# Kernel tuning notes

Measured on AMD Instinct MI355X. Metric: run time of the kernel, lower is better.

The kernel has to match this reference:

```python
import jax, jax.numpy as jnp
import numpy as np

EMBED_DIM = 128
NUM_HEADS = 4
WH, WW = 7, 7
N = WH * WW
HEAD_DIM = EMBED_DIM // NUM_HEADS
SCALE = HEAD_DIM ** -0.5


def _rel_position_index():
    # double_step_seq(2*Ww-1, Wh, 1, Ww), then idx = coords + coords.T, flip cols
    seq1 = np.arange(0, (2 * WW - 1) * WH, 2 * WW - 1)
    seq2 = np.arange(0, WW)
    coords = (seq1[:, None] + seq2[None, :]).reshape(1, -1)  # (1, N)
    idx = coords + coords.T                                   # (N, N)
    idx = idx[:, ::-1].copy()                                 # flip(1)
    return jnp.asarray(idx, dtype=jnp.int32)

REL_IDX = _rel_position_index()


def setup_inputs() -> dict:
    key = jax.random.key(0)
    ks = jax.random.split(key, 8)
    B = 4096
    nW = 64
    C = EMBED_DIM
    x = jax.random.normal(ks[0], (B, N, C), dtype=jnp.float32)
    # shift mask: values in (-inf, 0]; emulate with -100 on ~half the entries
    mask = jnp.where(jax.random.uniform(ks[1], (nW, N, N)) > 0.5, -100.0, 0.0).astype(jnp.float32)
    lim = 1.0 / np.sqrt(C)
    qkv_w = jax.random.uniform(ks[2], (3 * C, C), minval=-lim, maxval=lim, dtype=jnp.float32)
    qkv_b = jax.random.uniform(ks[3], (3 * C,), minval=-lim, maxval=lim, dtype=jnp.float32)
    proj_w = jax.random.uniform(ks[4], (C, C), minval=-lim, maxval=lim, dtype=jnp.float32)
    proj_b = jax.random.uniform(ks[5], (C,), minval=-lim, maxval=lim, dtype=jnp.float32)
    n_rel = (2 * WH - 1) * (2 * WW - 1)
    bias_table = 0.02 * jax.random.normal(ks[6], (n_rel, NUM_HEADS), dtype=jnp.float32)
    return {"x": x, "mask": mask, "qkv_w": qkv_w, "qkv_b": qkv_b,
            "proj_w": proj_w, "proj_b": proj_b, "bias_table": bias_table}


def reference(x, mask, qkv_w, qkv_b, proj_w, proj_b, bias_table):
    B, n, C = x.shape
    H, D = NUM_HEADS, HEAD_DIM
    qkv = x @ qkv_w.T + qkv_b                       # (B, N, 3C)
    qkv = qkv.reshape(B, n, 3, H, D).transpose(2, 0, 3, 1, 4)
    q, k, v = qkv[0], qkv[1], qkv[2]                # each (B, H, N, D)
    attn = jnp.einsum('bhnd,bhmd->bhnm', q * SCALE, k)
    # relative position bias gather: (N, N, H) -> (H, N, N)
    rel_bias = bias_table[REL_IDX.reshape(-1)].reshape(n, n, H).transpose(2, 0, 1)
    attn = attn + rel_bias[None]
    nW = mask.shape[0]
    attn = attn.reshape(B // nW, nW, H, n, n) + mask[None, :, None]
    attn = attn.reshape(B, H, n, n)
    attn = jax.nn.softmax(attn, axis=-1)
    out = jnp.einsum('bhnm,bhmd->bhnd', attn, v)    # (B, H, N, D)
    out = out.transpose(0, 2, 1, 3).reshape(B, n, C)
    return out @ proj_w.T + proj_b
```

## Files before the change

### kernel.cpp

```cpp
#include <hip/hip_runtime.h>


typedef __bf16 bf16_t;
typedef __bf16 bf8v  __attribute__((ext_vector_type(8)));
typedef __bf16 bf4v  __attribute__((ext_vector_type(4)));
typedef float  f4v   __attribute__((ext_vector_type(4)));

#define QK_SCALE 0.17677669529663687f

__device__ __forceinline__ f4v mfma16(bf8v a, bf8v b, f4v c) {
  return __builtin_amdgcn_mfma_f32_16x16x32_bf16(a, b, c, 0, 0, 0);
}

__device__ __forceinline__ bf8v join8(bf4v lo, bf4v hi) {
  return __builtin_shufflevector(lo, hi, 0, 1, 2, 3, 4, 5, 6, 7);
}

__global__ void prep_kernel(const float* __restrict__ mask,
                            const float* __restrict__ qkv_w,
                            const float* __restrict__ proj_w,
                            const float* __restrict__ bias_table,
                            bf16_t* __restrict__ wq,
                            bf16_t* __restrict__ wp,
                            float* __restrict__ cbs) {
  const int stride = gridDim.x * blockDim.x;
  const int tid0 = blockIdx.x * blockDim.x + threadIdx.x;
  for (int i = tid0; i < 24 * 4 * 64 * 8; i += stride) {
    int j = i & 7, l = (i >> 3) & 63, kt = (i >> 9) & 3, t = i >> 11;
    int n = t * 16 + (l & 15), k = kt * 32 + (l >> 4) * 8 + j;
    wq[i] = (bf16_t)qkv_w[n * 128 + k];
  }
  for (int i = tid0; i < 8 * 4 * 64 * 8; i += stride) {
    int j = i & 7, l = (i >> 3) & 63, kt = (i >> 9) & 3, t = i >> 11;
    int n = t * 16 + (l & 15), k = kt * 32 + (l >> 4) * 8 + j;
    wp[i] = (bf16_t)proj_w[n * 128 + k];
  }
  for (int i = tid0; i < 64 * 4 * 64 * 64; i += stride) {
    int j = i & 63;
    int l16 = j >> 2, nt = j & 3;
    int m = nt * 16 + l16;
    int n = (i >> 6) & 63, h = (i >> 12) & 3, w = i >> 14;
    float v;
    if (m >= 49) {
      v = -1e30f;
    } else if (n >= 49) {
      v = 0.0f;
    } else {
      int cn = 13 * (n / 7) + n % 7;
      int mm = 48 - m;
      int cm = 13 * (mm / 7) + mm % 7;
      v = bias_table[(cn + cm) * 4 + h] + mask[(w * 49 + n) * 49 + m];
    }
    cbs[i] = v;
  }
}

__global__ __launch_bounds__(256, 3) void msa_kernel(
    const float* __restrict__ x,
    const float* __restrict__ qkv_b,
    const float* __restrict__ proj_b,
    const bf16_t* __restrict__ wq,
    const bf16_t* __restrict__ wp,
    const float* __restrict__ cbs,
    float* __restrict__ out) {
  __shared__ __align__(16) bf16_t gA[8704];
  __shared__ __align__(16) bf16_t gB[4][4608];

#define AS(r, c)   gA[(r) * 136 + (c)]
#define VT(h, d, t) gA[((h) * 32 + (d)) * 68 + (t)]
#define QQ(h, r, d) gB[h][(r) * 36 + (d)]
#define KK(h, r, d) gB[h][2304 + (r) * 36 + (d)]
#define PP(h, n, m) gB[h][(n) * 72 + (m)]
#define OV(h, t, d) gB[h][(t) * 36 + (d)]

  const int tid = threadIdx.x;
  const int wv  = tid >> 6;
  const int ln  = tid & 63;
  const int l16 = ln & 15;
  const int l4  = ln >> 4;
  const int b   = blockIdx.x;
  const int w   = b & 63;

  {
    const float4* xb = (const float4*)(x + (size_t)b * (49 * 128));
    for (int i = tid; i < 64 * 32; i += 256) {
      int r = i >> 5, c4 = (i & 31) << 2;
      float4 v;
      if (r < 49) v = xb[(r * 128 + c4) >> 2];
      else        v = make_float4(0.f, 0.f, 0.f, 0.f);
      bf4v o = { (bf16_t)v.x, (bf16_t)v.y, (bf16_t)v.z, (bf16_t)v.w };
      *(bf4v*)&AS(r, c4) = o;
    }
  }
  __syncthreads();

  {
    f4v acc[4][6];
    for (int mt = 0; mt < 4; ++mt)
      for (int nj = 0; nj < 6; ++nj) acc[mt][nj] = (f4v){0.f, 0.f, 0.f, 0.f};
    for (int kt = 0; kt < 4; ++kt) {
      bf8v a[4];
      for (int mt = 0; mt < 4; ++mt)
        a[mt] = *(const bf8v*)&AS(mt * 16 + l16, kt * 32 + l4 * 8);
      bf8v bwv[6];
      for (int nj = 0; nj < 6; ++nj) {
        int t = wv * 6 + nj;
        bwv[nj] = *(const bf8v*)(wq + (((t * 4 + kt) * 64 + ln) << 3));
      }
      for (int mt = 0; mt < 4; ++mt)
        for (int nj = 0; nj < 6; ++nj)
          acc[mt][nj] = mfma16(a[mt], bwv[nj], acc[mt][nj]);
    }
    __syncthreads();
    for (int nj = 0; nj < 6; ++nj) {
      int t = wv * 6 + nj;
      int n0 = t * 16 + l16;
      float bias = qkv_b[n0];
      int sect = n0 >> 7;
      int h = (n0 & 127) >> 5;
      int d = n0 & 31;
      for (int mt = 0; mt < 4; ++mt) {
        int row0 = mt * 16 + l4 * 4;
        if (sect == 0) {
          for (int r = 0; r < 4; ++r)
            QQ(h, row0 + r, d) = (bf16_t)((acc[mt][nj][r] + bias) * QK_SCALE);
        } else if (sect == 1) {
          for (int r = 0; r < 4; ++r)
            KK(h, row0 + r, d) = (bf16_t)(acc[mt][nj][r] + bias);
        } else {
          bf4v o = { (bf16_t)(acc[mt][nj][0] + bias), (bf16_t)(acc[mt][nj][1] + bias),
                     (bf16_t)(acc[mt][nj][2] + bias), (bf16_t)(acc[mt][nj][3] + bias) };
          *(bf4v*)&VT(h, d, row0) = o;
        }
      }
    }
  }
  __syncthreads();

  {
    const int h = wv;
    f4v lg[4][4];
    bf8v qf[4], kf[4];
    for (int mt = 0; mt < 4; ++mt) {
      bf4v lo = *(const bf4v*)&QQ(h, mt * 16 + l16, l4 * 8);
      bf4v hi = *(const bf4v*)&QQ(h, mt * 16 + l16, l4 * 8 + 4);
      qf[mt] = join8(lo, hi);
    }
    for (int nt = 0; nt < 4; ++nt) {
      bf4v lo = *(const bf4v*)&KK(h, nt * 16 + l16, l4 * 8);
      bf4v hi = *(const bf4v*)&KK(h, nt * 16 + l16, l4 * 8 + 4);
      kf[nt] = join8(lo, hi);
    }
    for (int mt = 0; mt < 4; ++mt)
      for (int nt = 0; nt < 4; ++nt)
        lg[mt][nt] = mfma16(qf[mt], kf[nt], (f4v){0.f, 0.f, 0.f, 0.f});

    const float* cbp = cbs + ((size_t)(w * 4 + h) << 12);
    for (int mt = 0; mt < 4; ++mt) {
      for (int r = 0; r < 4; ++r) {
        int row = mt * 16 + l4 * 4 + r;
        float4 cbv = *(const float4*)(cbp + (row << 6) + l16 * 4);
        float vals[4];
        vals[0] = __expf(fmaxf(lg[mt][0][r] + cbv.x, -80.f));
        vals[1] = __expf(fmaxf(lg[mt][1][r] + cbv.y, -80.f));
        vals[2] = __expf(fmaxf(lg[mt][2][r] + cbv.z, -80.f));
        vals[3] = __expf(fmaxf(lg[mt][3][r] + cbv.w, -80.f));
        float s = (vals[0] + vals[1]) + (vals[2] + vals[3]);
        for (int off = 1; off < 16; off <<= 1) s += __shfl_xor(s, off);
        float inv = 1.0f / s;
        for (int nt = 0; nt < 4; ++nt)
          PP(h, row, nt * 16 + l16) = (bf16_t)(vals[nt] * inv);
      }
    }

    f4v oc[2][4];
    for (int mt = 0; mt < 2; ++mt)
      for (int nt = 0; nt < 4; ++nt) oc[mt][nt] = (f4v){0.f, 0.f, 0.f, 0.f};
    for (int ks = 0; ks < 2; ++ks) {
      bf8v vf[2], pf[4];
      for (int mt = 0; mt < 2; ++mt) {
        bf4v lo = *(const bf4v*)&VT(h, mt * 16 + l16, ks * 32 + l4 * 8);
        bf4v hi = *(const bf4v*)&VT(h, mt * 16 + l16, ks * 32 + l4 * 8 + 4);
        vf[mt] = join8(lo, hi);
      }
      for (int nt = 0; nt < 4; ++nt)
        pf[nt] = *(const bf8v*)&PP(h, nt * 16 + l16, ks * 32 + l4 * 8);
      for (int mt = 0; mt < 2; ++mt)
        for (int nt = 0; nt < 4; ++nt)
          oc[mt][nt] = mfma16(vf[mt], pf[nt], oc[mt][nt]);
    }
    for (int mt = 0; mt < 2; ++mt)
      for (int nt = 0; nt < 4; ++nt) {
        bf4v o = { (bf16_t)oc[mt][nt][0], (bf16_t)oc[mt][nt][1],
                   (bf16_t)oc[mt][nt][2], (bf16_t)oc[mt][nt][3] };
        *(bf4v*)&OV(h, nt * 16 + l16, mt * 16 + l4 * 4) = o;
      }
  }
  __syncthreads();

  {
    f4v acc[4][2];
    for (int mt = 0; mt < 4; ++mt)
      for (int nj = 0; nj < 2; ++nj) acc[mt][nj] = (f4v){0.f, 0.f, 0.f, 0.f};
    for (int kt = 0; kt < 4; ++kt) {
      bf8v a[4];
      for (int mt = 0; mt < 4; ++mt) {
        bf4v lo = *(const bf4v*)&OV(kt, mt * 16 + l16, l4 * 8);
        bf4v hi = *(const bf4v*)&OV(kt, mt * 16 + l16, l4 * 8 + 4);
        a[mt] = join8(lo, hi);
      }
      bf8v bwv[2];
      for (int nj = 0; nj < 2; ++nj) {
        int t = wv * 2 + nj;
        bwv[nj] = *(const bf8v*)(wp + (((t * 4 + kt) * 64 + ln) << 3));
      }
      for (int mt = 0; mt < 4; ++mt)
        for (int nj = 0; nj < 2; ++nj)
          acc[mt][nj] = mfma16(a[mt], bwv[nj], acc[mt][nj]);
    }
    float* ob = out + (size_t)b * (49 * 128);
    for (int nj = 0; nj < 2; ++nj) {
      int c = (wv * 2 + nj) * 16 + l16;
      float pb = proj_b[c];
      for (int mt = 0; mt < 4; ++mt) {
        for (int r = 0; r < 4; ++r) {
          int row = mt * 16 + l4 * 4 + r;
          if (row < 49) ob[row * 128 + c] = acc[mt][nj][r] + pb;
        }
      }
    }
  }
}

extern "C" void kernel_launch(void* const* d_in, const int* in_sizes, int n_in,
                              void* d_out, int out_size, void* d_ws, size_t ws_size,
                              hipStream_t stream) {
  const float* x          = (const float*)d_in[0];
  const float* mask       = (const float*)d_in[1];
  const float* qkv_w      = (const float*)d_in[2];
  const float* qkv_b      = (const float*)d_in[3];
  const float* proj_w     = (const float*)d_in[4];
  const float* proj_b     = (const float*)d_in[5];
  const float* bias_table = (const float*)d_in[6];

  char* ws = (char*)d_ws;
  bf16_t* wq = (bf16_t*)ws;
  bf16_t* wp = (bf16_t*)(ws + 98304);
  float*  cbs = (float*)(ws + 131072);

  prep_kernel<<<1024, 256, 0, stream>>>(mask, qkv_w, proj_w, bias_table, wq, wp, cbs);
  msa_kernel<<<4096, 256, 0, stream>>>(x, qkv_b, proj_b, wq, wp, cbs, (float*)d_out);
}
```

Baseline: 294.3 us.

## Make each wave compute its own head's QKV, removing block barriers and shrinking LDS

Each wave now computes Q, K and V projections only for its own head, reading x directly from global memory into bf16 MFMA fragments instead of staging it in shared memory. Per-head data lives in a wave-private LDS slice that is reused for Q, K, P and O, so only one block barrier remains, before the output projection. LDS use drops and occupancy is raised to 4 blocks per CU. The cost is that every wave re-reads x from global memory (and V needs a second pass), and the P·V product is split into two halves to fit the smaller buffer.

```diff
diff --git a/kernel.cpp b/kernel.cpp
--- a/kernel.cpp
+++ b/kernel.cpp
@@ -3,17 +3,12 @@
 
 typedef __bf16 bf16_t;
 typedef __bf16 bf8v  __attribute__((ext_vector_type(8)));
-typedef __bf16 bf4v  __attribute__((ext_vector_type(4)));
 typedef float  f4v   __attribute__((ext_vector_type(4)));
 
 #define QK_SCALE 0.17677669529663687f
 
 __device__ __forceinline__ f4v mfma16(bf8v a, bf8v b, f4v c) {
   return __builtin_amdgcn_mfma_f32_16x16x32_bf16(a, b, c, 0, 0, 0);
-}
-
-__device__ __forceinline__ bf8v join8(bf4v lo, bf4v hi) {
-  return __builtin_shufflevector(lo, hi, 0, 1, 2, 3, 4, 5, 6, 7);
 }
 
 __global__ void prep_kernel(const float* __restrict__ mask,
@@ -55,7 +50,7 @@
   }
 }
 
-__global__ __launch_bounds__(256, 3) void msa_kernel(
+__global__ __launch_bounds__(256, 4) void msa_kernel(
     const float* __restrict__ x,
     const float* __restrict__ qkv_b,
     const float* __restrict__ proj_b,
@@ -63,15 +58,10 @@
     const bf16_t* __restrict__ wp,
     const float* __restrict__ cbs,
     float* __restrict__ out) {
-  __shared__ __align__(16) bf16_t gA[8704];
-  __shared__ __align__(16) bf16_t gB[4][4608];
-
-#define AS(r, c)   gA[(r) * 136 + (c)]
-#define VT(h, d, t) gA[((h) * 32 + (d)) * 68 + (t)]
-#define QQ(h, r, d) gB[h][(r) * 36 + (d)]
-#define KK(h, r, d) gB[h][2304 + (r) * 36 + (d)]
-#define PP(h, n, m) gB[h][(n) * 72 + (m)]
-#define OV(h, t, d) gB[h][(t) * 36 + (d)]
+  __shared__ __align__(16) bf16_t sl[4][4864];
+
+#define TT(hh, r, c)  sl[hh][(r) * 40 + (c)]
+#define VTT(hh, d, m) sl[hh][2560 + (d) * 72 + (m)]
 
   const int tid = threadIdx.x;
   const int wv  = tid >> 6;
@@ -80,152 +70,211 @@
   const int l4  = ln >> 4;
   const int b   = blockIdx.x;
   const int w   = b & 63;
-
+  const int h   = wv;
+
+  const float* xb = x + (size_t)b * (49 * 128);
+
+  auto load_a = [&](int mt, int kt) -> bf8v {
+    int tok = mt * 16 + l16;
+    const float* p = xb + (tok < 49 ? tok * 128 : 0) + kt * 32 + l4 * 8;
+    float4 u0 = *(const float4*)p;
+    float4 u1 = *(const float4*)(p + 4);
+    if (tok >= 49) { u0 = make_float4(0.f, 0.f, 0.f, 0.f); u1 = u0; }
+    bf8v t = { (bf16_t)u0.x, (bf16_t)u0.y, (bf16_t)u0.z, (bf16_t)u0.w,
+               (bf16_t)u1.x, (bf16_t)u1.y, (bf16_t)u1.z, (bf16_t)u1.w };
+    return t;
+  };
+
+  f4v acc[4][4];
+#pragma unroll
+  for (int ti = 0; ti < 4; ++ti)
+#pragma unroll
+    for (int mt = 0; mt < 4; ++mt) acc[ti][mt] = (f4v){0.f, 0.f, 0.f, 0.f};
+#pragma unroll
+  for (int kt = 0; kt < 4; ++kt) {
+    bf8v a[4];
+#pragma unroll
+    for (int mt = 0; mt < 4; ++mt) a[mt] = load_a(mt, kt);
+    bf8v bb[4];
+#pragma unroll
+    for (int ti = 0; ti < 4; ++ti) {
+      int t = (ti < 2) ? (2 * h + ti) : (8 + 2 * h + (ti - 2));
+      bb[ti] = *(const bf8v*)(wq + (((t * 4 + kt) * 64 + ln) << 3));
+    }
+#pragma unroll
+    for (int ti = 0; ti < 4; ++ti)
+#pragma unroll
+      for (int mt = 0; mt < 4; ++mt)
+        acc[ti][mt] = mfma16(a[mt], bb[ti], acc[ti][mt]);
+  }
+
+  bf8v kf[4], qf[4];
+#pragma unroll
+  for (int ti = 0; ti < 2; ++ti) {
+    float bias = qkv_b[128 + 32 * h + ti * 16 + l16];
+#pragma unroll
+    for (int mt = 0; mt < 4; ++mt)
+#pragma unroll
+      for (int r = 0; r < 4; ++r)
+        TT(h, mt * 16 + l4 * 4 + r, ti * 16 + l16) = (bf16_t)(acc[2 + ti][mt][r] + bias);
+  }
+#pragma unroll
+  for (int mt = 0; mt < 4; ++mt)
+    kf[mt] = *(const bf8v*)&TT(h, mt * 16 + l16, l4 * 8);
+
+#pragma unroll
+  for (int ti = 0; ti < 2; ++ti) {
+    float bias = qkv_b[32 * h + ti * 16 + l16];
+#pragma unroll
+    for (int mt = 0; mt < 4; ++mt)
+#pragma unroll
+      for (int r = 0; r < 4; ++r)
+        TT(h, mt * 16 + l4 * 4 + r, ti * 16 + l16) =
+            (bf16_t)((acc[ti][mt][r] + bias) * QK_SCALE);
+  }
+#pragma unroll
+  for (int mt = 0; mt < 4; ++mt)
+    qf[mt] = *(const bf8v*)&TT(h, mt * 16 + l16, l4 * 8);
+
+  f4v vacc[2][4];
+#pragma unroll
+  for (int ti = 0; ti < 2; ++ti)
+#pragma unroll
+    for (int mt = 0; mt < 4; ++mt) vacc[ti][mt] = (f4v){0.f, 0.f, 0.f, 0.f};
+#pragma unroll
+  for (int kt = 0; kt < 4; ++kt) {
+    bf8v a[4];
+#pragma unroll
+    for (int mt = 0; mt < 4; ++mt) a[mt] = load_a(mt, kt);
+    bf8v bb[2];
+#pragma unroll
+    for (int ti = 0; ti < 2; ++ti) {
+      int t = 16 + 2 * h + ti;
+      bb[ti] = *(const bf8v*)(wq + (((t * 4 + kt) * 64 + ln) << 3));
+    }
+#pragma unroll
+    for (int ti = 0; ti < 2; ++ti)
+#pragma unroll
+      for (int mt = 0; mt < 4; ++mt)
+        vacc[ti][mt] = mfma16(a[mt], bb[ti], vacc[ti][mt]);
+  }
+#pragma unroll
+  for (int ti = 0; ti < 2; ++ti) {
+    float bias = qkv_b[256 + 32 * h + ti * 16 + l16];
+#pragma unroll
+    for (int mt = 0; mt < 4; ++mt)
+#pragma unroll
+      for (int r = 0; r < 4; ++r)
+        VTT(h, ti * 16 + l16, mt * 16 + l4 * 4 + r) = (bf16_t)(vacc[ti][mt][r] + bias);
+  }
+
+  f4v lg[4][4];
+#pragma unroll
+  for (int mt = 0; mt < 4; ++mt)
+#pragma unroll
+    for (int nt = 0; nt < 4; ++nt)
+      lg[mt][nt] = mfma16(qf[mt], kf[nt], (f4v){0.f, 0.f, 0.f, 0.f});
+
+  const float* cbp = cbs + ((size_t)(w * 4 + h) << 12);
+  float ph1[4][4][2];
+#pragma unroll
+  for (int mt = 0; mt < 4; ++mt) {
+#pragma unroll
+    for (int r = 0; r < 4; ++r) {
+      int row = mt * 16 + l4 * 4 + r;
+      float4 cbv = *(const float4*)(cbp + (row << 6) + l16 * 4);
+      float v0 = __expf(fmaxf(lg[mt][0][r] + cbv.x, -80.f));
+      float v1 = __expf(fmaxf(lg[mt][1][r] + cbv.y, -80.f));
+      float v2 = __expf(fmaxf(lg[mt][2][r] + cbv.z, -80.f));
+      float v3 = __expf(fmaxf(lg[mt][3][r] + cbv.w, -80.f));
+      float s = (v0 + v1) + (v2 + v3);
+#pragma unroll
+      for (int off = 1; off < 16; off <<= 1) s += __shfl_xor(s, off);
+      float inv = 1.0f / s;
+      TT(h, row, l16)      = (bf16_t)(v0 * inv);
+      TT(h, row, 16 + l16) = (bf16_t)(v1 * inv);
+      ph1[mt][r][0] = v2 * inv;
+      ph1[mt][r][1] = v3 * inv;
+    }
+  }
+
+  f4v oc[4][2];
+#pragma unroll
+  for (int nt = 0; nt < 4; ++nt)
+#pragma unroll
+    for (int dt = 0; dt < 2; ++dt) oc[nt][dt] = (f4v){0.f, 0.f, 0.f, 0.f};
   {
-    const float4* xb = (const float4*)(x + (size_t)b * (49 * 128));
-    for (int i = tid; i < 64 * 32; i += 256) {
-      int r = i >> 5, c4 = (i & 31) << 2;
-      float4 v;
-      if (r < 49) v = xb[(r * 128 + c4) >> 2];
-      else        v = make_float4(0.f, 0.f, 0.f, 0.f);
-      bf4v o = { (bf16_t)v.x, (bf16_t)v.y, (bf16_t)v.z, (bf16_t)v.w };
-      *(bf4v*)&AS(r, c4) = o;
-    }
-  }
+    bf8v pf[4], vf[2];
+#pragma unroll
+    for (int nt = 0; nt < 4; ++nt) pf[nt] = *(const bf8v*)&TT(h, nt * 16 + l16, l4 * 8);
+#pragma unroll
+    for (int dt = 0; dt < 2; ++dt) vf[dt] = *(const bf8v*)&VTT(h, dt * 16 + l16, l4 * 8);
+#pragma unroll
+    for (int nt = 0; nt < 4; ++nt)
+#pragma unroll
+      for (int dt = 0; dt < 2; ++dt) oc[nt][dt] = mfma16(pf[nt], vf[dt], oc[nt][dt]);
+#pragma unroll
+    for (int mt = 0; mt < 4; ++mt)
+#pragma unroll
+      for (int r = 0; r < 4; ++r) {
+        int row = mt * 16 + l4 * 4 + r;
+        TT(h, row, l16)      = (bf16_t)ph1[mt][r][0];
+        TT(h, row, 16 + l16) = (bf16_t)ph1[mt][r][1];
+      }
+#pragma unroll
+    for (int nt = 0; nt < 4; ++nt) pf[nt] = *(const bf8v*)&TT(h, nt * 16 + l16, l4 * 8);
+#pragma unroll
+    for (int dt = 0; dt < 2; ++dt) vf[dt] = *(const bf8v*)&VTT(h, dt * 16 + l16, 32 + l4 * 8);
+#pragma unroll
+    for (int nt = 0; nt < 4; ++nt)
+#pragma unroll
+      for (int dt = 0; dt < 2; ++dt) oc[nt][dt] = mfma16(pf[nt], vf[dt], oc[nt][dt]);
+  }
+#pragma unroll
+  for (int nt = 0; nt < 4; ++nt)
+#pragma unroll
+    for (int dt = 0; dt < 2; ++dt)
+#pragma unroll
+      for (int r = 0; r < 4; ++r)
+        TT(h, nt * 16 + l4 * 4 + r, dt * 16 + l16) = (bf16_t)(oc[nt][dt][r]);
+
   __syncthreads();
 
   {
-    f4v acc[4][6];
-    for (int mt = 0; mt < 4; ++mt)
-      for (int nj = 0; nj < 6; ++nj) acc[mt][nj] = (f4v){0.f, 0.f, 0.f, 0.f};
+    f4v pacc[4][2];
+#pragma unroll
+    for (int mt = 0; mt < 4; ++mt)
+#pragma unroll
+      for (int nj = 0; nj < 2; ++nj) pacc[mt][nj] = (f4v){0.f, 0.f, 0.f, 0.f};
+#pragma unroll
     for (int kt = 0; kt < 4; ++kt) {
       bf8v a[4];
+#pragma unroll
       for (int mt = 0; mt < 4; ++mt)
-        a[mt] = *(const bf8v*)&AS(mt * 16 + l16, kt * 32 + l4 * 8);
-      bf8v bwv[6];
-      for (int nj = 0; nj < 6; ++nj) {
-        int t = wv * 6 + nj;
-        bwv[nj] = *(const bf8v*)(wq + (((t * 4 + kt) * 64 + ln) << 3));
-      }
-      for (int mt = 0; mt < 4; ++mt)
-        for (int nj = 0; nj < 6; ++nj)
-          acc[mt][nj] = mfma16(a[mt], bwv[nj], acc[mt][nj]);
-    }
-    __syncthreads();
-    for (int nj = 0; nj < 6; ++nj) {
-      int t = wv * 6 + nj;
-      int n0 = t * 16 + l16;
-      float bias = qkv_b[n0];
-      int sect = n0 >> 7;
-      int h = (n0 & 127) >> 5;
-      int d = n0 & 31;
-      for (int mt = 0; mt < 4; ++mt) {
-        int row0 = mt * 16 + l4 * 4;
-        if (sect == 0) {
-          for (int r = 0; r < 4; ++r)
-            QQ(h, row0 + r, d) = (bf16_t)((acc[mt][nj][r] + bias) * QK_SCALE);
-        } else if (sect == 1) {
-          for (int r = 0; r < 4; ++r)
-            KK(h, row0 + r, d) = (bf16_t)(acc[mt][nj][r] + bias);
-        } else {
-          bf4v o = { (bf16_t)(acc[mt][nj][0] + bias), (bf16_t)(acc[mt][nj][1] + bias),
-                     (bf16_t)(acc[mt][nj][2] + bias), (bf16_t)(acc[mt][nj][3] + bias) };
-          *(bf4v*)&VT(h, d, row0) = o;
-        }
-      }
-    }
-  }
-  __syncthreads();
-
-  {
-    const int h = wv;
-    f4v lg[4][4];
-    bf8v qf[4], kf[4];
-    for (int mt = 0; mt < 4; ++mt) {
-      bf4v lo = *(const bf4v*)&QQ(h, mt * 16 + l16, l4 * 8);
-      bf4v hi = *(const bf4v*)&QQ(h, mt * 16 + l16, l4 * 8 + 4);
-      qf[mt] = join8(lo, hi);
-    }
-    for (int nt = 0; nt < 4; ++nt) {
-      bf4v lo = *(const bf4v*)&KK(h, nt * 16 + l16, l4 * 8);
-      bf4v hi = *(const bf4v*)&KK(h, nt * 16 + l16, l4 * 8 + 4);
-      kf[nt] = join8(lo, hi);
-    }
-    for (int mt = 0; mt < 4; ++mt)
-      for (int nt = 0; nt < 4; ++nt)
-        lg[mt][nt] = mfma16(qf[mt], kf[nt], (f4v){0.f, 0.f, 0.f, 0.f});
-
-    const float* cbp = cbs + ((size_t)(w * 4 + h) << 12);
-    for (int mt = 0; mt < 4; ++mt) {
-      for (int r = 0; r < 4; ++r) {
-        int row = mt * 16 + l4 * 4 + r;
-        float4 cbv = *(const float4*)(cbp + (row << 6) + l16 * 4);
-        float vals[4];
-        vals[0] = __expf(fmaxf(lg[mt][0][r] + cbv.x, -80.f));
-        vals[1] = __expf(fmaxf(lg[mt][1][r] + cbv.y, -80.f));
-        vals[2] = __expf(fmaxf(lg[mt][2][r] + cbv.z, -80.f));
-        vals[3] = __expf(fmaxf(lg[mt][3][r] + cbv.w, -80.f));
-        float s = (vals[0] + vals[1]) + (vals[2] + vals[3]);
-        for (int off = 1; off < 16; off <<= 1) s += __shfl_xor(s, off);
-        float inv = 1.0f / s;
-        for (int nt = 0; nt < 4; ++nt)
-          PP(h, row, nt * 16 + l16) = (bf16_t)(vals[nt] * inv);
-      }
-    }
-
-    f4v oc[2][4];
-    for (int mt = 0; mt < 2; ++mt)
-      for (int nt = 0; nt < 4; ++nt) oc[mt][nt] = (f4v){0.f, 0.f, 0.f, 0.f};
-    for (int ks = 0; ks < 2; ++ks) {
-      bf8v vf[2], pf[4];
-      for (int mt = 0; mt < 2; ++mt) {
-        bf4v lo = *(const bf4v*)&VT(h, mt * 16 + l16, ks * 32 + l4 * 8);
-        bf4v hi = *(const bf4v*)&VT(h, mt * 16 + l16, ks * 32 + l4 * 8 + 4);
-        vf[mt] = join8(lo, hi);
-      }
-      for (int nt = 0; nt < 4; ++nt)
-        pf[nt] = *(const bf8v*)&PP(h, nt * 16 + l16, ks * 32 + l4 * 8);
-      for (int mt = 0; mt < 2; ++mt)
-        for (int nt = 0; nt < 4; ++nt)
-          oc[mt][nt] = mfma16(vf[mt], pf[nt], oc[mt][nt]);
-    }
-    for (int mt = 0; mt < 2; ++mt)
-      for (int nt = 0; nt < 4; ++nt) {
-        bf4v o = { (bf16_t)oc[mt][nt][0], (bf16_t)oc[mt][nt][1],
-                   (bf16_t)oc[mt][nt][2], (bf16_t)oc[mt][nt][3] };
-        *(bf4v*)&OV(h, nt * 16 + l16, mt * 16 + l4 * 4) = o;
-      }
-  }
-  __syncthreads();
-
-  {
-    f4v acc[4][2];
-    for (int mt = 0; mt < 4; ++mt)
-      for (int nj = 0; nj < 2; ++nj) acc[mt][nj] = (f4v){0.f, 0.f, 0.f, 0.f};
-    for (int kt = 0; kt < 4; ++kt) {
-      bf8v a[4];
-      for (int mt = 0; mt < 4; ++mt) {
-        bf4v lo = *(const bf4v*)&OV(kt, mt * 16 + l16, l4 * 8);
-        bf4v hi = *(const bf4v*)&OV(kt, mt * 16 + l16, l4 * 8 + 4);
-        a[mt] = join8(lo, hi);
-      }
+        a[mt] = *(const bf8v*)&TT(kt, mt * 16 + l16, l4 * 8);
       bf8v bwv[2];
+#pragma unroll
       for (int nj = 0; nj < 2; ++nj) {
         int t = wv * 2 + nj;
         bwv[nj] = *(const bf8v*)(wp + (((t * 4 + kt) * 64 + ln) << 3));
       }
+#pragma unroll
       for (int mt = 0; mt < 4; ++mt)
+#pragma unroll
         for (int nj = 0; nj < 2; ++nj)
-          acc[mt][nj] = mfma16(a[mt], bwv[nj], acc[mt][nj]);
+          pacc[mt][nj] = mfma16(a[mt], bwv[nj], pacc[mt][nj]);
     }
     float* ob = out + (size_t)b * (49 * 128);
+#pragma unroll
     for (int nj = 0; nj < 2; ++nj) {
       int c = (wv * 2 + nj) * 16 + l16;
       float pb = proj_b[c];
+#pragma unroll
       for (int mt = 0; mt < 4; ++mt) {
+#pragma unroll
         for (int r = 0; r < 4; ++r) {
           int row = mt * 16 + l4 * 4 + r;
-          if (row < 49) ob[row * 128 + c] = acc[mt][nj][r] + pb;
+          if (row < 49) ob[row * 128 + c] = pacc[mt][nj][r] + pb;
         }
       }
     }
```

Result: slower. 317.0 us (+7.7%).
